# Optimization experiments

Measured on AMD Instinct MI355X. Metric: run time of the kernel, lower is better.

Reference implementation:

```python
import jax, jax.numpy as jnp
import numpy as np

B, N, M, D, H = 4, 1024, 1024, 1024, 16
HD = D // H
MH = int(D * 4.0 * 2 / 3)  # SwiGLU hidden = 2730
EPS = 1e-6


def setup_inputs() -> dict:
    key = jax.random.key(0)
    ks = jax.random.split(key, 16)
    w = lambda k, shape: jax.random.normal(k, shape, jnp.float32) * 0.02
    return dict(
        x=jax.random.normal(ks[0], (B, N, D), jnp.float32),
        source_tokens=jax.random.normal(ks[1], (B, M, D), jnp.float32),
        c=jax.random.normal(ks[2], (B, D), jnp.float32),
        ada_w=w(ks[3], (D, 9 * D)), ada_b=jnp.zeros((9 * D,), jnp.float32),
        n1_w=jnp.ones((D,), jnp.float32), nc_w=jnp.ones((D,), jnp.float32), n2_w=jnp.ones((D,), jnp.float32),
        sa_qkv_w=w(ks[4], (D, 3 * D)), sa_qkv_b=jnp.zeros((3 * D,), jnp.float32),
        sa_qn_w=jnp.ones((HD,), jnp.float32), sa_kn_w=jnp.ones((HD,), jnp.float32),
        sa_o_w=w(ks[5], (D, D)), sa_o_b=jnp.zeros((D,), jnp.float32),
        ca_q_w=w(ks[6], (D, D)), ca_q_b=jnp.zeros((D,), jnp.float32),
        ca_kv_w=w(ks[7], (D, 2 * D)), ca_kv_b=jnp.zeros((2 * D,), jnp.float32),
        ca_qn_w=jnp.ones((HD,), jnp.float32), ca_kn_w=jnp.ones((HD,), jnp.float32),
        ca_o_w=w(ks[8], (D, D)), ca_o_b=jnp.zeros((D,), jnp.float32),
        mlp_w1=w(ks[9], (D, MH)), mlp_b1=jnp.zeros((MH,), jnp.float32),
        mlp_w2=w(ks[10], (D, MH)), mlp_b2=jnp.zeros((MH,), jnp.float32),
        mlp_w3=w(ks[11], (MH, D)), mlp_b3=jnp.zeros((D,), jnp.float32),
    )


def _rms(x, w):
    return x * jax.lax.rsqrt(jnp.mean(x * x, axis=-1, keepdims=True) + EPS) * w


def _modulate(x, shift, scale):
    return x * (1.0 + scale[:, None, :]) + shift[:, None, :]


def _sdpa(q, k, v):
    # q: (B,Nq,H,HD), k/v: (B,Nk,H,HD)
    s = jnp.einsum('bqhd,bkhd->bhqk', q, k) * (HD ** -0.5)
    a = jax.nn.softmax(s, axis=-1)
    o = jnp.einsum('bhqk,bkhd->bqhd', a, v)
    return o.reshape(q.shape[0], q.shape[1], D)


def reference(x, source_tokens, c, ada_w, ada_b, n1_w, nc_w, n2_w,
              sa_qkv_w, sa_qkv_b, sa_qn_w, sa_kn_w, sa_o_w, sa_o_b,
              ca_q_w, ca_q_b, ca_kv_w, ca_kv_b, ca_qn_w, ca_kn_w, ca_o_w, ca_o_b,
              mlp_w1, mlp_b1, mlp_w2, mlp_b2, mlp_w3, mlp_b3):
    mods = jax.nn.silu(c) @ ada_w + ada_b
    (shift_sa, scale_sa, gate_sa, shift_ca, scale_ca, gate_ca,
     shift_ff, scale_ff, gate_ff) = jnp.split(mods, 9, axis=-1)

    # --- self-attention sublayer ---
    xn = _modulate(_rms(x, n1_w), shift_sa, scale_sa)
    qkv = xn @ sa_qkv_w + sa_qkv_b
    q, k, v = jnp.split(qkv, 3, axis=-1)
    q = _rms(q.reshape(B, N, H, HD), sa_qn_w)
    k = _rms(k.reshape(B, N, H, HD), sa_kn_w)
    v = v.reshape(B, N, H, HD)
    attn = _sdpa(q, k, v) @ sa_o_w + sa_o_b
    x = x + gate_sa[:, None, :] * attn

    # --- cross-attention sublayer ---
    xn = _modulate(_rms(x, nc_w), shift_ca, scale_ca)
    q = (xn @ ca_q_w + ca_q_b).reshape(B, N, H, HD)
    kv = source_tokens @ ca_kv_w + ca_kv_b
    k, v = jnp.split(kv, 2, axis=-1)
    q = _rms(q, ca_qn_w)
    k = _rms(k.reshape(B, M, H, HD), ca_kn_w)
    v = v.reshape(B, M, H, HD)
    cattn = _sdpa(q, k, v) @ ca_o_w + ca_o_b
    x = x + gate_ca[:, None, :] * cattn

    # --- SwiGLU FFN sublayer ---
    xn = _modulate(_rms(x, n2_w), shift_ff, scale_ff)
    ff = (jax.nn.silu(xn @ mlp_w1 + mlp_b1) * (xn @ mlp_w2 + mlp_b2)) @ mlp_w3 + mlp_b3
    x = x + gate_ff[:, None, :] * ff
    return x
```

## Files before the change

### kernel.cpp

```cpp
#include <hip/hip_runtime.h>

typedef unsigned short u16;
typedef __attribute__((ext_vector_type(8))) short short8;
typedef __attribute__((ext_vector_type(4))) float f32x4;

#define DD 1024
#define NN 1024
#define MODS_LD 9216

__device__ __forceinline__ float bf2f(u16 v) {
  unsigned int u = ((unsigned int)v) << 16;
  return __builtin_bit_cast(float, u);
}
__device__ __forceinline__ u16 f2bf(float f) {
  unsigned int u = __builtin_bit_cast(unsigned int, f);
  unsigned int lsb = (u >> 16) & 1;
  u += 0x7fffu + lsb;
  return (u16)(u >> 16);
}
__device__ __forceinline__ unsigned cvtpk_bf16(float a, float b) {
  unsigned r;
  asm volatile("v_cvt_pk_bf16_f32 %0, %1, %2" : "=v"(r) : "v"(a), "v"(b));
  return r;
}
__device__ __forceinline__ float exp2x(float x) {
  float r;
  asm("v_exp_f32 %0, %1" : "=v"(r) : "v"(x));
  return r;
}

__device__ __forceinline__ void gload_lds16(const u16* g, u16* l) {
  __builtin_amdgcn_global_load_lds(
      (const __attribute__((address_space(1))) unsigned int*)g,
      (__attribute__((address_space(3))) unsigned int*)l, 16, 0, 0);
}

__device__ __forceinline__ void xcd_tile(int ncolChunks, int cr, int cc, int& tm, int& tn) {
  int id = blockIdx.x;
  int c = id & 7, i = id >> 3;
  int chunkRow = c / ncolChunks, chunkCol = c % ncolChunks;
  tm = chunkRow * cr + (i % cr);
  tn = chunkCol * cc + (i / cr);
}

struct TDesc {
  const float* s;
  u16* d;
  int R, C, R2, C2, gx, start;
};
struct TPack {
  TDesc t[8];
};

__global__ void transpose_all(TPack p) {
  __shared__ float tile[32][33];
  int id = blockIdx.x;
  int k = 0;
#pragma unroll
  for (int j = 1; j < 8; ++j)
    if (id >= p.t[j].start) k = j;
  const float* src = p.t[k].s;
  u16* dst = p.t[k].d;
  int R = p.t[k].R, C = p.t[k].C, R2 = p.t[k].R2, C2 = p.t[k].C2;
  int rem = id - p.t[k].start;
  int gx = p.t[k].gx;
  int r0 = (rem % gx) * 32, c0 = (rem / gx) * 32;
  int tx = threadIdx.x, ty = threadIdx.y;
#pragma unroll
  for (int i = 0; i < 4; ++i) {
    int r = r0 + ty + i * 8, c = c0 + tx;
    tile[ty + i * 8][tx] = (r < R && c < C) ? src[(long)r * C + c] : 0.f;
  }
  __syncthreads();
#pragma unroll
  for (int i = 0; i < 4; ++i) {
    int c = c0 + ty + i * 8, r = r0 + tx;
    if (c < C2 && r < R2) dst[(long)c * R2 + r] = f2bf(tile[tx][ty + i * 8]);
  }
}

__global__ void cvt_bf16_kernel(const float* __restrict__ in, u16* __restrict__ out, long n4) {
  long i = (long)blockIdx.x * 256 + threadIdx.x;
  if (i >= n4) return;
  float4 v = *(const float4*)&in[i * 4];
  ushort4 pk = {f2bf(v.x), f2bf(v.y), f2bf(v.z), f2bf(v.w)};
  *(ushort4*)&out[i * 4] = pk;
}

#define MODS_KS 32
__global__ __launch_bounds__(256) void mods_partial(const float* __restrict__ c,
                                                    const float* __restrict__ aw,
                                                    float* __restrict__ part) {
  __shared__ float scs[4][32];
  int j = blockIdx.x * 256 + threadIdx.x;
  int ks = blockIdx.y;
  int d0 = ks * (DD / MODS_KS);
  int t = threadIdx.x;
  if (t < 32) {
#pragma unroll
    for (int b2 = 0; b2 < 4; ++b2) {
      float v = c[b2 * DD + d0 + t];
      scs[b2][t] = v / (1.f + __expf(-v));
    }
  }
  __syncthreads();
  float a0 = 0.f, a1 = 0.f, a2 = 0.f, a3 = 0.f;
#pragma unroll 8
  for (int d = 0; d < DD / MODS_KS; ++d) {
    float w = aw[(long)(d0 + d) * MODS_LD + j];
    a0 = fmaf(scs[0][d], w, a0);
    a1 = fmaf(scs[1][d], w, a1);
    a2 = fmaf(scs[2][d], w, a2);
    a3 = fmaf(scs[3][d], w, a3);
  }
  long base = (long)ks * 4 * MODS_LD + j;
  part[base] = a0;
  part[base + MODS_LD] = a1;
  part[base + 2 * MODS_LD] = a2;
  part[base + 3 * MODS_LD] = a3;
}

__global__ __launch_bounds__(256) void mods_reduce(const float* __restrict__ part,
                                                   const float* __restrict__ ab,
                                                   float* __restrict__ mods) {
  int j = blockIdx.x * 256 + threadIdx.x;
  int b = blockIdx.y;
  float acc = ab[j];
#pragma unroll
  for (int ks = 0; ks < MODS_KS; ++ks) acc += part[((long)ks * 4 + b) * MODS_LD + j];
  mods[(long)b * MODS_LD + j] = acc;
}

__global__ __launch_bounds__(256) void rmsmod_kernel(const float* __restrict__ x,
                                                     const float* __restrict__ w,
                                                     const float* __restrict__ mods,
                                                     int shiftOff, int scaleOff,
                                                     u16* __restrict__ out) {
  long row = blockIdx.x;
  int b = (int)(row >> 10);
  int t = threadIdx.x;
  const float* xr = x + row * DD;
  float4 v = *(const float4*)&xr[t * 4];
  float ss = v.x * v.x + v.y * v.y + v.z * v.z + v.w * v.w;
#pragma unroll
  for (int msk = 1; msk < 64; msk <<= 1) ss += __shfl_xor(ss, msk);
  __shared__ float red[4];
  if ((t & 63) == 0) red[t >> 6] = ss;
  __syncthreads();
  float tot = red[0] + red[1] + red[2] + red[3];
  float inv = rsqrtf(tot * (1.f / DD) + 1e-6f);
  const float* mrow = mods + (long)b * MODS_LD;
  float vv[4] = {v.x, v.y, v.z, v.w};
  u16 tmp[4];
#pragma unroll
  for (int j = 0; j < 4; ++j) {
    int c = t * 4 + j;
    float rr = vv[j] * inv * w[c] * (1.f + mrow[scaleOff + c]) + mrow[shiftOff + c];
    tmp[j] = f2bf(rr);
  }
  ushort4 pk = {tmp[0], tmp[1], tmp[2], tmp[3]};
  *(ushort4*)&out[row * DD + t * 4] = pk;
}

template <int MODE, int BN, int MINW, int NORM, int VT>
__global__ __launch_bounds__(256, MINW) void gemm_bf16(
    const u16* __restrict__ A, const u16* __restrict__ Bt, int K, int ldc,
    const float* __restrict__ bias, int biasN, u16* __restrict__ outb,
    float* __restrict__ outf, const float* __restrict__ xin,
    const float* __restrict__ mods, int gateOff, int ncolChunks, int cr, int cc,
    const float* __restrict__ nw, int normLo, int normHi, float nscale,
    u16* __restrict__ vtOut, int vLo, int vHi, int vOff) {
  constexpr int WC = BN / 2;
  constexpr int NT = WC / 16;
  constexpr int LOADS = 4 + BN / 32;
  __shared__ u16 As[2][128 * 64];
  __shared__ u16 Bs[2][BN * 64];
  int t = threadIdx.x;
  int l = t & 63, w = t >> 6;
  int wr = w >> 1, wc = w & 1;
  int lg = l >> 4, ll = l & 15;
  int rx = ll & 7;
  int tm, tn;
  xcd_tile(ncolChunks, cr, cc, tm, tn);
  long rowTile = (long)tm * 128;
  long colTile = (long)tn * BN;
  const u16* Ap = A + rowTile * K;
  const u16* Bp = Bt + colTile * K;
  int srow = t >> 3;
  int sck = ((t & 7) ^ (srow & 7)) * 8;

  auto stage = [&](int buf, int k0) {
#pragma unroll
    for (int i = 0; i < 4; ++i)
      gload_lds16(Ap + (long)(i * 32 + srow) * K + k0 + sck, &As[buf][(i * 256 + t) * 8]);
#pragma unroll
    for (int i = 0; i < BN / 32; ++i)
      gload_lds16(Bp + (long)(i * 32 + srow) * K + k0 + sck, &Bs[buf][(i * 256 + t) * 8]);
  };

  const int ntk = K >> 6;
  stage(0, 0);
  if (ntk > 1) stage(1, 64);

  f32x4 acc[4][NT] = {};
  int cur = 0;
  for (int i = 0; i < ntk; ++i) {
    if (i + 1 < ntk) {
      asm volatile("s_waitcnt vmcnt(%0)" ::"i"(LOADS) : "memory");
    } else {
      asm volatile("s_waitcnt vmcnt(0)" ::: "memory");
    }
    __builtin_amdgcn_s_barrier();
    const u16* Ac = As[cur];
    const u16* Bc = Bs[cur];
    short8 af[2][4], bfr[2][NT];
#pragma unroll
    for (int kk = 0; kk < 2; ++kk) {
#pragma unroll
      for (int m2 = 0; m2 < 4; ++m2)
        af[kk][m2] =
            *(const short8*)&Ac[(wr * 64 + m2 * 16 + ll) * 64 + (((kk * 4 + lg) ^ rx) << 3)];
#pragma unroll
      for (int n2 = 0; n2 < NT; ++n2)
        bfr[kk][n2] =
            *(const short8*)&Bc[(wc * WC + n2 * 16 + ll) * 64 + (((kk * 4 + lg) ^ rx) << 3)];
    }
    asm volatile("s_waitcnt lgkmcnt(0)" ::: "memory");
    __builtin_amdgcn_sched_barrier(0);
    __builtin_amdgcn_s_barrier();
    if (i + 2 < ntk) stage(cur, (i + 2) * 64);
    __builtin_amdgcn_s_setprio(1);
#pragma unroll
    for (int kk = 0; kk < 2; ++kk)
#pragma unroll
      for (int m2 = 0; m2 < 4; ++m2)
#pragma unroll
        for (int n2 = 0; n2 < NT; ++n2)
          acc[m2][n2] = __builtin_amdgcn_mfma_f32_16x16x32_bf16(af[kk][m2], bfr[kk][n2],
                                                                acc[m2][n2], 0, 0, 0);
    __builtin_amdgcn_s_setprio(0);
    cur ^= 1;
  }

  if (NORM == 1 && tn >= normLo && tn < normHi) {
    float bv[NT], wnv[NT];
#pragma unroll
    for (int n2 = 0; n2 < NT; ++n2) {
      long cg = colTile + wc * WC + n2 * 16 + ll;
      bv[n2] = bias[cg];
      wnv[n2] = nw[n2 * 16 + ll];
    }
#pragma unroll
    for (int m2 = 0; m2 < 4; ++m2) {
#pragma unroll
      for (int r = 0; r < 4; ++r) {
        float vals[NT];
        float ss = 0.f;
#pragma unroll
        for (int n2 = 0; n2 < NT; ++n2) {
          vals[n2] = acc[m2][n2][r] + bv[n2];
          ss += vals[n2] * vals[n2];
        }
        ss += __shfl_xor(ss, 1);
        ss += __shfl_xor(ss, 2);
        ss += __shfl_xor(ss, 4);
        ss += __shfl_xor(ss, 8);
        float inv = rsqrtf(ss * (1.f / 64) + 1e-6f) * nscale;
        long rg = rowTile + wr * 64 + m2 * 16 + lg * 4 + r;
#pragma unroll
        for (int n2 = 0; n2 < NT; ++n2) {
          long cg = colTile + wc * WC + n2 * 16 + ll;
          outb[rg * ldc + cg] = f2bf(vals[n2] * inv * wnv[n2]);
        }
      }
    }
    return;
  }

  if (VT == 1 && tn >= vLo && tn < vHi) {
    int bblk = (int)(rowTile >> 10);
    int tokBase = (int)(rowTile & 1023) + wr * 64;
    int hGlob = (int)((colTile + wc * WC - vOff) >> 6);
    long vBase = ((long)(bblk * 16 + hGlob) * 64) * 1024;
    u16* scr = &As[0][0] + w * 1152;
#pragma unroll
    for (int n2 = 0; n2 < NT; ++n2) {
      long cg = colTile + wc * WC + n2 * 16 + ll;
      float bv = bias[cg];
#pragma unroll
      for (int m2 = 0; m2 < 4; ++m2)
#pragma unroll
        for (int r = 0; r < 4; ++r)
          scr[ll * 72 + m2 * 16 + lg * 4 + r] = f2bf(acc[m2][n2][r] + bv);
      asm volatile("s_waitcnt lgkmcnt(0)" ::: "memory");
      __builtin_amdgcn_sched_barrier(0);
      int dloc = l >> 2, tko = (l & 3) * 16;
      short8 v0 = *(const short8*)&scr[dloc * 72 + tko];
      short8 v1 = *(const short8*)&scr[dloc * 72 + tko + 8];
      asm volatile("s_waitcnt lgkmcnt(0)" ::: "memory");
      __builtin_amdgcn_sched_barrier(0);
      u16* dst = vtOut + vBase + (long)(n2 * 16 + dloc) * 1024 + tokBase + tko;
      *(short8*)dst = v0;
      *(short8*)(dst + 8) = v1;
    }
    return;
  }

#pragma unroll
  for (int n2 = 0; n2 < NT; ++n2) {
    long cg = colTile + wc * WC + n2 * 16 + ll;
    float bv = (cg < biasN) ? bias[cg] : 0.f;
#pragma unroll
    for (int m2 = 0; m2 < 4; ++m2) {
#pragma unroll
      for (int r = 0; r < 4; ++r) {
        long rg = rowTile + wr * 64 + m2 * 16 + lg * 4 + r;
        float v = acc[m2][n2][r] + bv;
        long idx = rg * ldc + cg;
        if (MODE == 0) {
          outb[idx] = f2bf(v);
        } else {
          int bb = (int)(rg >> 10);
          outf[idx] = xin[idx] + mods[(long)bb * MODS_LD + gateOff + cg] * v;
        }
      }
    }
  }
}

__global__ __launch_bounds__(256, 2) void gemm_dual_swiglu(
    const u16* __restrict__ A, const u16* __restrict__ B1t, const u16* __restrict__ B2t,
    int K, int ldc, const float* __restrict__ b1, const float* __restrict__ b2, int biasN,
    u16* __restrict__ outb, int ncolChunks, int cr, int cc) {
  constexpr int BN = 64, WC = 32, NT = 2;
  __shared__ u16 As[2][128 * 64];
  __shared__ u16 B1s[2][BN * 64];
  __shared__ u16 B2s[2][BN * 64];
  int t = threadIdx.x;
  int l = t & 63, w = t >> 6;
  int wr = w >> 1, wc = w & 1;
  int lg = l >> 4, ll = l & 15;
  int rx = ll & 7;
  int tm, tn;
  xcd_tile(ncolChunks, cr, cc, tm, tn);
  long rowTile = (long)tm * 128;
  long colTile = (long)tn * BN;
  const u16* Ap = A + rowTile * K;
  const u16* B1p = B1t + colTile * K;
  const u16* B2p = B2t + colTile * K;
  int srow = t >> 3;
  int sck = ((t & 7) ^ (srow & 7)) * 8;

  auto stage = [&](int buf, int k0) {
#pragma unroll
    for (int i = 0; i < 4; ++i)
      gload_lds16(Ap + (long)(i * 32 + srow) * K + k0 + sck, &As[buf][(i * 256 + t) * 8]);
#pragma unroll
    for (int i = 0; i < 2; ++i) {
      gload_lds16(B1p + (long)(i * 32 + srow) * K + k0 + sck, &B1s[buf][(i * 256 + t) * 8]);
      gload_lds16(B2p + (long)(i * 32 + srow) * K + k0 + sck, &B2s[buf][(i * 256 + t) * 8]);
    }
  };

  const int ntk = K >> 6;
  stage(0, 0);
  if (ntk > 1) stage(1, 64);

  f32x4 acc1[4][NT] = {}, acc2[4][NT] = {};
  int cur = 0;
  for (int i = 0; i < ntk; ++i) {
    if (i + 1 < ntk) {
      asm volatile("s_waitcnt vmcnt(8)" ::: "memory");
    } else {
      asm volatile("s_waitcnt vmcnt(0)" ::: "memory");
    }
    __builtin_amdgcn_s_barrier();
    const u16* Ac = As[cur];
    const u16* B1c = B1s[cur];
    const u16* B2c = B2s[cur];
    short8 af[2][4], b1f[2][NT], b2f[2][NT];
#pragma unroll
    for (int kk = 0; kk < 2; ++kk) {
#pragma unroll
      for (int m2 = 0; m2 < 4; ++m2)
        af[kk][m2] =
            *(const short8*)&Ac[(wr * 64 + m2 * 16 + ll) * 64 + (((kk * 4 + lg) ^ rx) << 3)];
#pragma unroll
      for (int n2 = 0; n2 < NT; ++n2) {
        int off = (wc * WC + n2 * 16 + ll) * 64 + (((kk * 4 + lg) ^ rx) << 3);
        b1f[kk][n2] = *(const short8*)&B1c[off];
        b2f[kk][n2] = *(const short8*)&B2c[off];
      }
    }
    asm volatile("s_waitcnt lgkmcnt(0)" ::: "memory");
    __builtin_amdgcn_sched_barrier(0);
    __builtin_amdgcn_s_barrier();
    if (i + 2 < ntk) stage(cur, (i + 2) * 64);
    __builtin_amdgcn_s_setprio(1);
#pragma unroll
    for (int kk = 0; kk < 2; ++kk)
#pragma unroll
      for (int m2 = 0; m2 < 4; ++m2)
#pragma unroll
        for (int n2 = 0; n2 < NT; ++n2) {
          acc1[m2][n2] = __builtin_amdgcn_mfma_f32_16x16x32_bf16(af[kk][m2], b1f[kk][n2],
                                                                 acc1[m2][n2], 0, 0, 0);
          acc2[m2][n2] = __builtin_amdgcn_mfma_f32_16x16x32_bf16(af[kk][m2], b2f[kk][n2],
                                                                 acc2[m2][n2], 0, 0, 0);
        }
    __builtin_amdgcn_s_setprio(0);
    cur ^= 1;
  }
#pragma unroll
  for (int n2 = 0; n2 < NT; ++n2) {
    long cg = colTile + wc * WC + n2 * 16 + ll;
    float bv1 = (cg < biasN) ? b1[cg] : 0.f;
    float bv2 = (cg < biasN) ? b2[cg] : 0.f;
#pragma unroll
    for (int m2 = 0; m2 < 4; ++m2) {
#pragma unroll
      for (int r = 0; r < 4; ++r) {
        long rg = rowTile + wr * 64 + m2 * 16 + lg * 4 + r;
        float v1 = acc1[m2][n2][r] + bv1;
        float v2 = acc2[m2][n2][r] + bv2;
        float sg = v1 / (1.f + __expf(-v1));
        outb[rg * ldc + cg] = f2bf(sg * v2);
      }
    }
  }
}

__global__ __launch_bounds__(512, 2) void attn_kernel(
    const u16* __restrict__ qb, int qStride, const u16* __restrict__ kb, int kvStride,
    const u16* __restrict__ vt, const float* __restrict__ qn, u16* __restrict__ outp,
    int Nk, int Mpb) {
  __shared__ u16 Qs[128 * 64];
  __shared__ u16 Ks[2][64 * 64];
  __shared__ u16 Vs[2][64 * 64];
  __shared__ u16 Ps[8][16 * 64];
  int t = threadIdx.x, w = t >> 6, l = t & 63;
  int h = blockIdx.x, b = blockIdx.y, qt = blockIdx.z;
  int lg = l >> 4, ll = l & 15;
  int rx = ll & 7;

  const u16* Qbase = qb + ((long)(b * NN + qt * 128)) * qStride + h * 64;
  const u16* Kbase = kb + ((long)b * Mpb) * kvStride + h * 64;
  const u16* Vbase = vt + ((long)(b * 16 + h) * 64) * 1024;

  int srow = t >> 3;
  int schunk = t & 7;

#pragma unroll
  for (int sh = 0; sh < 2; ++sh) {
    int row = sh * 64 + srow;
    int ck = schunk ^ (row & 7);
    gload_lds16(Qbase + (long)row * qStride + ck * 8, &Qs[sh * 4096 + t * 8]);
  }
  auto stageKV = [&](int buf, int kt) {
    const u16* kn = Kbase + (long)kt * 64 * kvStride;
    const u16* vn = Vbase + kt * 64;
    int ck = schunk ^ (srow & 7);
    gload_lds16(kn + (long)srow * kvStride + ck * 8, &Ks[buf][t * 8]);
    gload_lds16(vn + (long)srow * 1024 + ck * 8, &Vs[buf][t * 8]);
  };
  const int ntk = Nk >> 6;
  stageKV(0, 0);
  if (ntk > 1) stageKV(1, 1);

  short8 qf0, qf1;
  float mrun = -1e30f, ssum = 0.f;
  f32x4 o[4] = {};

  int cur = 0;
  for (int kt = 0; kt < ntk; ++kt) {
    if (kt + 1 < ntk) {
      asm volatile("s_waitcnt vmcnt(2)" ::: "memory");
    } else {
      asm volatile("s_waitcnt vmcnt(0)" ::: "memory");
    }
    __builtin_amdgcn_s_barrier();
    if (kt == 0) {
      qf0 = *(const short8*)&Qs[(w * 16 + ll) * 64 + ((lg ^ rx) << 3)];
      qf1 = *(const short8*)&Qs[(w * 16 + ll) * 64 + (((4 + lg) ^ rx) << 3)];
      float qv0[8], qv1[8], ss = 0.f;
#pragma unroll
      for (int j = 0; j < 8; ++j) {
        qv0[j] = bf2f((u16)qf0[j]);
        qv1[j] = bf2f((u16)qf1[j]);
        ss += qv0[j] * qv0[j] + qv1[j] * qv1[j];
      }
      ss += __shfl_xor(ss, 16);
      ss += __shfl_xor(ss, 32);
      float inv = rsqrtf(ss * (1.f / 64) + 1e-6f) * (0.125f * 1.44269504f);
      int d0 = (lg ^ rx) << 3, d1 = ((4 + lg) ^ rx) << 3;
      u16 t0[8], t1[8];
#pragma unroll
      for (int j = 0; j < 8; ++j) {
        t0[j] = f2bf(qv0[j] * inv * qn[d0 + j]);
        t1[j] = f2bf(qv1[j] * inv * qn[d1 + j]);
      }
      qf0 = *(short8*)t0;
      qf1 = *(short8*)t1;
    }
    const u16* Kc = Ks[cur];
    f32x4 s[4] = {};
#pragma unroll
    for (int n = 0; n < 4; ++n) {
      short8 kf0 = *(const short8*)&Kc[(n * 16 + ll) * 64 + ((lg ^ rx) << 3)];
      short8 kf1 = *(const short8*)&Kc[(n * 16 + ll) * 64 + (((4 + lg) ^ rx) << 3)];
      s[n] = __builtin_amdgcn_mfma_f32_16x16x32_bf16(kf0, qf0, s[n], 0, 0, 0);
      s[n] = __builtin_amdgcn_mfma_f32_16x16x32_bf16(kf1, qf1, s[n], 0, 0, 0);
    }
    float t0 = fmaxf(fmaxf(s[0][0], s[0][1]), fmaxf(s[0][2], s[0][3]));
    float t1 = fmaxf(fmaxf(s[1][0], s[1][1]), fmaxf(s[1][2], s[1][3]));
    float t2 = fmaxf(fmaxf(s[2][0], s[2][1]), fmaxf(s[2][2], s[2][3]));
    float t3 = fmaxf(fmaxf(s[3][0], s[3][1]), fmaxf(s[3][2], s[3][3]));
    float pm = fmaxf(fmaxf(t0, t1), fmaxf(t2, t3));
    pm = fmaxf(pm, __shfl_xor(pm, 16));
    pm = fmaxf(pm, __shfl_xor(pm, 32));
    bool resc = !__all(pm - mrun <= 8.f);
    float nm = resc ? fmaxf(mrun, pm) : mrun;
    float pn[4][4];
#pragma unroll
    for (int n = 0; n < 4; ++n)
#pragma unroll
      for (int r = 0; r < 4; ++r) pn[n][r] = exp2x(s[n][r] - nm);
    float r0 = (pn[0][0] + pn[0][1]) + (pn[0][2] + pn[0][3]);
    float r1 = (pn[1][0] + pn[1][1]) + (pn[1][2] + pn[1][3]);
    float r2 = (pn[2][0] + pn[2][1]) + (pn[2][2] + pn[2][3]);
    float r3 = (pn[3][0] + pn[3][1]) + (pn[3][2] + pn[3][3]);
    float rs = (r0 + r1) + (r2 + r3);
    rs += __shfl_xor(rs, 16);
    rs += __shfl_xor(rs, 32);
    if (resc) {
      float alpha = exp2x(mrun - nm);
      ssum = ssum * alpha + rs;
      float a0 = __shfl(alpha, lg * 4 + 0);
      float a1 = __shfl(alpha, lg * 4 + 1);
      float a2 = __shfl(alpha, lg * 4 + 2);
      float a3 = __shfl(alpha, lg * 4 + 3);
#pragma unroll
      for (int n = 0; n < 4; ++n) {
        o[n][0] *= a0;
        o[n][1] *= a1;
        o[n][2] *= a2;
        o[n][3] *= a3;
      }
    } else {
      ssum += rs;
    }
    mrun = nm;
#pragma unroll
    for (int n = 0; n < 4; ++n) {
      uint2 pkd;
      pkd.x = cvtpk_bf16(pn[n][0], pn[n][1]);
      pkd.y = cvtpk_bf16(pn[n][2], pn[n][3]);
      int gran = n * 2 + (lg >> 1);
      int perm = gran ^ rx;
      *(uint2*)&Ps[w][ll * 64 + perm * 8 + (lg & 1) * 4] = pkd;
    }
    short8 pf0 = *(const short8*)&Ps[w][ll * 64 + ((lg ^ rx) << 3)];
    short8 pf1 = *(const short8*)&Ps[w][ll * 64 + (((4 + lg) ^ rx) << 3)];
    const u16* Vc = Vs[cur];
    short8 vfr[4][2];
#pragma unroll
    for (int n = 0; n < 4; ++n) {
      vfr[n][0] = *(const short8*)&Vc[(n * 16 + ll) * 64 + ((lg ^ rx) << 3)];
      vfr[n][1] = *(const short8*)&Vc[(n * 16 + ll) * 64 + (((4 + lg) ^ rx) << 3)];
    }
    asm volatile("s_waitcnt lgkmcnt(0)" ::: "memory");
    __builtin_amdgcn_sched_barrier(0);
    __builtin_amdgcn_s_barrier();
    if (kt + 2 < ntk) stageKV(cur, kt + 2);
    __builtin_amdgcn_s_setprio(1);
#pragma unroll
    for (int n = 0; n < 4; ++n) {
      o[n] = __builtin_amdgcn_mfma_f32_16x16x32_bf16(pf0, vfr[n][0], o[n], 0, 0, 0);
      o[n] = __builtin_amdgcn_mfma_f32_16x16x32_bf16(pf1, vfr[n][1], o[n], 0, 0, 0);
    }
    __builtin_amdgcn_s_setprio(0);
    cur ^= 1;
  }
  float s0 = __shfl(ssum, lg * 4 + 0);
  float s1 = __shfl(ssum, lg * 4 + 1);
  float s2 = __shfl(ssum, lg * 4 + 2);
  float s3 = __shfl(ssum, lg * 4 + 3);
  float i0 = 1.f / s0, i1 = 1.f / s1, i2 = 1.f / s2, i3 = 1.f / s3;
#pragma unroll
  for (int n = 0; n < 4; ++n) {
    float ir[4] = {i0, i1, i2, i3};
#pragma unroll
    for (int r = 0; r < 4; ++r) {
      long row = (long)b * NN + qt * 128 + w * 16 + lg * 4 + r;
      int col = h * 64 + n * 16 + ll;
      outp[row * DD + col] = f2bf(o[n][r] * ir[r]);
    }
  }
}

extern "C" void kernel_launch(void* const* d_in, const int* in_sizes, int n_in,
                              void* d_out, int out_size, void* d_ws, size_t ws_size,
                              hipStream_t stream) {
  const float* x = (const float*)d_in[0];
  const float* src = (const float*)d_in[1];
  const float* c = (const float*)d_in[2];
  const float* ada_w = (const float*)d_in[3];
  const float* ada_b = (const float*)d_in[4];
  const float* n1_w = (const float*)d_in[5];
  const float* nc_w = (const float*)d_in[6];
  const float* n2_w = (const float*)d_in[7];
  const float* sa_qkv_w = (const float*)d_in[8];
  const float* sa_qkv_b = (const float*)d_in[9];
  const float* sa_qn_w = (const float*)d_in[10];
  const float* sa_kn_w = (const float*)d_in[11];
  const float* sa_o_w = (const float*)d_in[12];
  const float* sa_o_b = (const float*)d_in[13];
  const float* ca_q_w = (const float*)d_in[14];
  const float* ca_q_b = (const float*)d_in[15];
  const float* ca_kv_w = (const float*)d_in[16];
  const float* ca_kv_b = (const float*)d_in[17];
  const float* ca_qn_w = (const float*)d_in[18];
  const float* ca_kn_w = (const float*)d_in[19];
  const float* ca_o_w = (const float*)d_in[20];
  const float* ca_o_b = (const float*)d_in[21];
  const float* mlp_w1 = (const float*)d_in[22];
  const float* mlp_b1 = (const float*)d_in[23];
  const float* mlp_w2 = (const float*)d_in[24];
  const float* mlp_b2 = (const float*)d_in[25];
  const float* mlp_w3 = (const float*)d_in[26];
  const float* mlp_b3 = (const float*)d_in[27];
  float* out = (float*)d_out;

  char* p = (char*)d_ws;
  auto alloc = [&](size_t bytes) {
    char* r = p;
    p += (bytes + 255) & ~(size_t)255;
    return r;
  };
  float* mods = (float*)alloc(4l * 9216 * 4);
  float* part = (float*)alloc((long)MODS_KS * 4 * 9216 * 4);
  u16* qkvT = (u16*)alloc(3072l * 1024 * 2);
  u16* saoT = (u16*)alloc(1024l * 1024 * 2);
  u16* caqT = (u16*)alloc(1024l * 1024 * 2);
  u16* cakvT = (u16*)alloc(2048l * 1024 * 2);
  u16* caoT = (u16*)alloc(1024l * 1024 * 2);
  u16* w1T = (u16*)alloc(2816l * 1024 * 2);
  u16* w2T = (u16*)alloc(2816l * 1024 * 2);
  u16* w3T = (u16*)alloc(1024l * 2816 * 2);
  u16* xnb = (u16*)alloc(4096l * 1024 * 2);
  u16* srcb = (u16*)alloc(4096l * 1024 * 2);
  u16* bufA = (u16*)alloc(4096l * 3072 * 2);
  u16* bufB = (u16*)alloc(4096l * 2048 * 2);
  u16* attO = (u16*)alloc(4096l * 1024 * 2);
  u16* vtb = (u16*)alloc(4096l * 1024 * 2);

  TPack tp;
  tp.t[0] = {sa_qkv_w, qkvT, 1024, 3072, 1024, 3072, 32, 0};
  tp.t[1] = {sa_o_w, saoT, 1024, 1024, 1024, 1024, 32, 3072};
  tp.t[2] = {ca_q_w, caqT, 1024, 1024, 1024, 1024, 32, 4096};
  tp.t[3] = {ca_kv_w, cakvT, 1024, 2048, 1024, 2048, 32, 5120};
  tp.t[4] = {ca_o_w, caoT, 1024, 1024, 1024, 1024, 32, 7168};
  tp.t[5] = {mlp_w1, w1T, 1024, 2730, 1024, 2816, 32, 8192};
  tp.t[6] = {mlp_w2, w2T, 1024, 2730, 1024, 2816, 32, 11008};
  tp.t[7] = {mlp_w3, w3T, 2730, 1024, 2816, 1024, 88, 13824};
  transpose_all<<<16640, dim3(32, 8), 0, stream>>>(tp);
  cvt_bf16_kernel<<<4096, 256, 0, stream>>>(src, srcb, 4096l * 1024 / 4);
  mods_partial<<<dim3(36, MODS_KS), 256, 0, stream>>>(c, ada_w, part);
  mods_reduce<<<dim3(36, 4), 256, 0, stream>>>(part, ada_b, mods);

  rmsmod_kernel<<<4096, 256, 0, stream>>>(x, n1_w, mods, 0, 1024, xnb);
  gemm_bf16<0, 128, 2, 1, 1><<<768, 256, 0, stream>>>(
      xnb, qkvT, 1024, 3072, sa_qkv_b, 3072, bufA, nullptr, nullptr, nullptr, 0, 4, 16, 6,
      sa_kn_w, 8, 16, 1.0f, vtb, 16, 24, 2048);
  attn_kernel<<<dim3(16, 4, 8), 512, 0, stream>>>(bufA, 3072, bufA + 1024, 3072, vtb, sa_qn_w,
                                                  attO, 1024, 1024);
  gemm_bf16<1, 64, 3, 0, 0><<<512, 256, 0, stream>>>(
      attO, saoT, 1024, 1024, sa_o_b, 1024, nullptr, out, x, mods, 2048, 2, 8, 8, nullptr, 0,
      0, 0.f, nullptr, 0, 0, 0);

  rmsmod_kernel<<<4096, 256, 0, stream>>>(out, nc_w, mods, 3072, 4096, xnb);
  gemm_bf16<0, 64, 3, 0, 0><<<512, 256, 0, stream>>>(
      xnb, caqT, 1024, 1024, ca_q_b, 1024, bufA, nullptr, nullptr, nullptr, 0, 2, 8, 8,
      nullptr, 0, 0, 0.f, nullptr, 0, 0, 0);
  gemm_bf16<0, 128, 2, 1, 1><<<512, 256, 0, stream>>>(
      srcb, cakvT, 1024, 2048, ca_kv_b, 2048, bufB, nullptr, nullptr, nullptr, 0, 2, 8, 8,
      ca_kn_w, 0, 8, 1.0f, vtb, 8, 16, 1024);
  attn_kernel<<<dim3(16, 4, 8), 512, 0, stream>>>(bufA, 1024, bufB, 2048, vtb, ca_qn_w, attO,
                                                  1024, 1024);
  gemm_bf16<1, 64, 3, 0, 0><<<512, 256, 0, stream>>>(
      attO, caoT, 1024, 1024, ca_o_b, 1024, nullptr, out, out, mods, 5120, 2, 8, 8, nullptr,
      0, 0, 0.f, nullptr, 0, 0, 0);

  rmsmod_kernel<<<4096, 256, 0, stream>>>(out, n2_w, mods, 6144, 7168, xnb);
  gemm_dual_swiglu<<<1408, 256, 0, stream>>>(xnb, w1T, w2T, 1024, 2816, mlp_b1, mlp_b2, 2730,
                                             bufA, 4, 16, 11);
  gemm_bf16<1, 64, 3, 0, 0><<<512, 256, 0, stream>>>(
      bufA, w3T, 2816, 1024, mlp_b3, 1024, nullptr, out, out, mods, 8192, 2, 8, 8, nullptr, 0,
      0, 0.f, nullptr, 0, 0, 0);
}
```

Before: 322.7 us.

## Load SwiGLU second weight operand directly to registers, bypassing LDS

In the dual SwiGLU GEMM, the W2 tile is no longer staged through shared memory. Each wave loads its own B2 fragments straight from global memory into registers one k-step ahead, using a ping-pong pair of register buffers and a loop manually unrolled by two. This cuts LDS footprint and traffic so launch bounds can be raised to 3 blocks per CU. The cost is uncoalesced-ish direct global loads whose latency must be hidden by the prefetch, plus higher register pressure. The loop assumes an even k-tile count.

Result: slower. 373.2 us (+15.7%).

```diff
diff --git a/kernel.cpp b/kernel.cpp
--- a/kernel.cpp
+++ b/kernel.cpp
@@ -328,14 +328,55 @@
   }
 }
 
-__global__ __launch_bounds__(256, 2) void gemm_dual_swiglu(
+#define DITER(CS, NS, I)                                                            \
+  {                                                                                 \
+    if ((I) + 1 < ntk) {                                                            \
+      asm volatile("s_waitcnt vmcnt(6)" ::: "memory");                              \
+    } else {                                                                        \
+      asm volatile("s_waitcnt vmcnt(0)" ::: "memory");                              \
+    }                                                                               \
+    __builtin_amdgcn_s_barrier();                                                   \
+    const u16* Ac = As[cur];                                                        \
+    const u16* B1c = B1s[cur];                                                      \
+    short8 af[2][4], b1f[2][2];                                                     \
+    _Pragma("unroll") for (int kk = 0; kk < 2; ++kk) {                              \
+      _Pragma("unroll") for (int m2 = 0; m2 < 4; ++m2) af[kk][m2] =                 \
+          *(const short8*)&Ac[(wr * 64 + m2 * 16 + ll) * 64 +                       \
+                              (((kk * 4 + lg) ^ rx) << 3)];                         \
+      _Pragma("unroll") for (int n2 = 0; n2 < 2; ++n2) b1f[kk][n2] =                \
+          *(const short8*)&B1c[(wc * 32 + n2 * 16 + ll) * 64 +                      \
+                               (((kk * 4 + lg) ^ rx) << 3)];                        \
+    }                                                                               \
+    asm volatile("s_waitcnt lgkmcnt(0)" ::: "memory");                              \
+    __builtin_amdgcn_sched_barrier(0);                                              \
+    __builtin_amdgcn_s_barrier();                                                   \
+    if ((I) + 1 < ntk) {                                                            \
+      _Pragma("unroll") for (int kk = 0; kk < 2; ++kk)                              \
+          _Pragma("unroll") for (int n2 = 0; n2 < 2; ++n2)                          \
+              NS[kk * 2 + n2] = *(const short8*)(B2l + (long)n2 * 16 * K +          \
+                                                 ((I) + 1) * 64 + kk * 32);         \
+    }                                                                               \
+    if ((I) + 2 < ntk) stage(cur, ((I) + 2) * 64);                                  \
+    __builtin_amdgcn_s_setprio(1);                                                  \
+    _Pragma("unroll") for (int kk = 0; kk < 2; ++kk)                                \
+        _Pragma("unroll") for (int m2 = 0; m2 < 4; ++m2)                            \
+            _Pragma("unroll") for (int n2 = 0; n2 < 2; ++n2) {                      \
+      acc1[m2][n2] = __builtin_amdgcn_mfma_f32_16x16x32_bf16(                       \
+          af[kk][m2], b1f[kk][n2], acc1[m2][n2], 0, 0, 0);                          \
+      acc2[m2][n2] = __builtin_amdgcn_mfma_f32_16x16x32_bf16(                       \
+          af[kk][m2], CS[kk * 2 + n2], acc2[m2][n2], 0, 0, 0);                      \
+    }                                                                               \
+    __builtin_amdgcn_s_setprio(0);                                                  \
+    cur ^= 1;                                                                       \
+  }
+
+__global__ __launch_bounds__(256, 3) void gemm_dual_swiglu(
     const u16* __restrict__ A, const u16* __restrict__ B1t, const u16* __restrict__ B2t,
     int K, int ldc, const float* __restrict__ b1, const float* __restrict__ b2, int biasN,
     u16* __restrict__ outb, int ncolChunks, int cr, int cc) {
   constexpr int BN = 64, WC = 32, NT = 2;
   __shared__ u16 As[2][128 * 64];
   __shared__ u16 B1s[2][BN * 64];
-  __shared__ u16 B2s[2][BN * 64];
   int t = threadIdx.x;
   int l = t & 63, w = t >> 6;
   int wr = w >> 1, wc = w & 1;
@@ -356,60 +397,27 @@
     for (int i = 0; i < 4; ++i)
       gload_lds16(Ap + (long)(i * 32 + srow) * K + k0 + sck, &As[buf][(i * 256 + t) * 8]);
 #pragma unroll
-    for (int i = 0; i < 2; ++i) {
+    for (int i = 0; i < 2; ++i)
       gload_lds16(B1p + (long)(i * 32 + srow) * K + k0 + sck, &B1s[buf][(i * 256 + t) * 8]);
-      gload_lds16(B2p + (long)(i * 32 + srow) * K + k0 + sck, &B2s[buf][(i * 256 + t) * 8]);
-    }
   };
 
+  const u16* B2l = B2p + (long)(wc * WC + ll) * K + lg * 8;
   const int ntk = K >> 6;
+
   stage(0, 0);
+  short8 b2a[4], b2b[4];
+#pragma unroll
+  for (int kk = 0; kk < 2; ++kk)
+#pragma unroll
+    for (int n2 = 0; n2 < 2; ++n2)
+      b2a[kk * 2 + n2] = *(const short8*)(B2l + (long)n2 * 16 * K + kk * 32);
   if (ntk > 1) stage(1, 64);
 
   f32x4 acc1[4][NT] = {}, acc2[4][NT] = {};
   int cur = 0;
-  for (int i = 0; i < ntk; ++i) {
-    if (i + 1 < ntk) {
-      asm volatile("s_waitcnt vmcnt(8)" ::: "memory");
-    } else {
-      asm volatile("s_waitcnt vmcnt(0)" ::: "memory");
-    }
-    __builtin_amdgcn_s_barrier();
-    const u16* Ac = As[cur];
-    const u16* B1c = B1s[cur];
-    const u16* B2c = B2s[cur];
-    short8 af[2][4], b1f[2][NT], b2f[2][NT];
-#pragma unroll
-    for (int kk = 0; kk < 2; ++kk) {
-#pragma unroll
-      for (int m2 = 0; m2 < 4; ++m2)
-        af[kk][m2] =
-            *(const short8*)&Ac[(wr * 64 + m2 * 16 + ll) * 64 + (((kk * 4 + lg) ^ rx) << 3)];
-#pragma unroll
-      for (int n2 = 0; n2 < NT; ++n2) {
-        int off = (wc * WC + n2 * 16 + ll) * 64 + (((kk * 4 + lg) ^ rx) << 3);
-        b1f[kk][n2] = *(const short8*)&B1c[off];
-        b2f[kk][n2] = *(const short8*)&B2c[off];
-      }
-    }
-    asm volatile("s_waitcnt lgkmcnt(0)" ::: "memory");
-    __builtin_amdgcn_sched_barrier(0);
-    __builtin_amdgcn_s_barrier();
-    if (i + 2 < ntk) stage(cur, (i + 2) * 64);
-    __builtin_amdgcn_s_setprio(1);
-#pragma unroll
-    for (int kk = 0; kk < 2; ++kk)
-#pragma unroll
-      for (int m2 = 0; m2 < 4; ++m2)
-#pragma unroll
-        for (int n2 = 0; n2 < NT; ++n2) {
-          acc1[m2][n2] = __builtin_amdgcn_mfma_f32_16x16x32_bf16(af[kk][m2], b1f[kk][n2],
-                                                                 acc1[m2][n2], 0, 0, 0);
-          acc2[m2][n2] = __builtin_amdgcn_mfma_f32_16x16x32_bf16(af[kk][m2], b2f[kk][n2],
-                                                                 acc2[m2][n2], 0, 0, 0);
-        }
-    __builtin_amdgcn_s_setprio(0);
-    cur ^= 1;
+  for (int i = 0; i < ntk; i += 2) {
+    DITER(b2a, b2b, i);
+    DITER(b2b, b2a, i + 1);
   }
 #pragma unroll
   for (int n2 = 0; n2 < NT; ++n2) {
```
